# Kernel optimization log

Measured on AMD Instinct MI355X. Metric: run time of the kernel, lower is better.

## Reference

```python
import jax, jax.numpy as jnp
import numpy as np

B, IN_DIM, N_NODES, N_LEAVES, N_ACTIONS = 131072, 128, 511, 512, 16


def setup_inputs() -> dict:
    key = jax.random.key(0)
    k1, k2, k3, k4 = jax.random.split(key, 4)
    x = jax.random.normal(k1, (B, IN_DIM), dtype=jnp.float32)
    W1 = jax.random.normal(k2, (N_NODES, IN_DIM), dtype=jnp.float32) * 0.1
    b1 = jax.random.normal(k3, (N_NODES,), dtype=jnp.float32) * 0.1
    W2 = jax.random.normal(k4, (N_LEAVES, 2 * N_NODES), dtype=jnp.float32) * 0.05
    # leaf -> action assignment; arange % n_actions guarantees every group non-empty
    leaf_actions = (jnp.arange(N_LEAVES) % N_ACTIONS).astype(jnp.int32)
    return {"x": x, "W1": W1, "b1": b1, "W2": W2, "leaf_actions": leaf_actions}


def reference(x, W1, b1, W2, leaf_actions):
    # linear1
    h = x @ W1.T + b1                      # [B, N_NODES]
    # relu(h) || relu(-h)
    z = jnp.concatenate([jax.nn.relu(h), jax.nn.relu(-h)], axis=1)  # [B, 2*N_NODES]
    # linear2 (no bias)
    y = z @ W2.T                           # [B, N_LEAVES]
    # grouped segment-max over leaf columns, grouped by action id
    pooled = jax.ops.segment_max(y.T, leaf_actions, num_segments=N_ACTIONS).T  # [B, N_ACTIONS]
    return jax.nn.softmax(pooled, axis=-1)
```

## Files before the change

kernel.cpp:

```cpp
#include <hip/hip_runtime.h>
#include <hip/hip_bf16.h>

typedef unsigned short u16;
typedef unsigned int u32;
typedef __attribute__((ext_vector_type(8))) short bf16x8;
typedef __attribute__((ext_vector_type(16))) float f32x16;

#define NROWS   131072
#define KDIM    128
#define NNODES  511
#define NACT    16

__device__ __forceinline__ u16 f2b(float v) {
  return __builtin_bit_cast(u16, __float2bfloat16(v));
}

union Frag {
  bf16x8 v;
  u16    u[8];
  int4   i;
  int    d[4];
};

#define Z16 {0.f,0.f,0.f,0.f,0.f,0.f,0.f,0.f,0.f,0.f,0.f,0.f,0.f,0.f,0.f,0.f}

__global__ void prep_k(const float* __restrict__ W1, const float* __restrict__ W2,
                       const float* __restrict__ b1, u16* __restrict__ w1f,
                       u16* __restrict__ wgt, float* __restrict__ b1r) {
  int bid = blockIdx.x, t = threadIdx.x;
  if (bid < 256) {
    int o = bid * 256 + t;
    int j = o & 7, l = (o >> 3) & 63, ks = (o >> 9) & 7, nt = o >> 12;
    int node = nt * 32 + (l & 31);
    int k = ks * 16 + ((l >> 5) << 3) + j;
    w1f[o] = f2b(node < NNODES ? W1[node * KDIM + k] : 0.f);
  } else if (bid < 2304) {
    int o = (bid - 256) * 256 + t;
    int j = o & 7, l = (o >> 3) & 63, lt = (o >> 9) & 15, s = o >> 13;
    int type = s & 1, kstep = s >> 1;
    int leaf = lt * 32 + (l & 31);
    int n = kstep * 16 + ((l >> 5) << 3) + j;
    float va = 0.f, vb = 0.f;
    if (n < NNODES) {
      va = W2[leaf * (2 * NNODES) + n];
      vb = W2[leaf * (2 * NNODES) + NNODES + n];
    }
    wgt[o] = f2b(type ? 0.5f * (va + vb) : 0.5f * (va - vb));
  } else {
    int o = (bid - 2304) * 256 + t;
    int r = o & 15, hi2 = (o >> 4) & 1, nt = o >> 5;
    int node = nt * 32 + (r & 3) + 8 * (r >> 2) + 4 * hi2;
    b1r[o] = (node < NNODES) ? b1[node] : 0.f;
  }
}

__global__ __launch_bounds__(512, 2) void fused_k(const float* __restrict__ x,
                                                  const u16* __restrict__ w1f,
                                                  const u16* __restrict__ wgt,
                                                  const float* __restrict__ b1r,
                                                  float* __restrict__ out) {
  __shared__ u16 Hh[4 * 32 * 64 * 8];
  __shared__ u16 Ss[32 * 64 * 8];

  const int t = threadIdx.x, w = t >> 6, l = t & 63;
  const int la = l & 31, hi = l >> 5;
  const int rg = blockIdx.x;

  {
    const float* xb = x + (size_t)rg * 128 * KDIM;
#pragma unroll
    for (int i = 0; i < 4; ++i) {
      int f = w * 4 + i;
      int rt = f >> 3, ks = f & 7;
      const float* src = xb + (rt * 32 + la) * KDIM + ks * 16 + hi * 8;
      float4 v0 = *(const float4*)src;
      float4 v1 = *(const float4*)(src + 4);
      Frag fr;
      fr.u[0] = f2b(v0.x); fr.u[1] = f2b(v0.y); fr.u[2] = f2b(v0.z); fr.u[3] = f2b(v0.w);
      fr.u[4] = f2b(v1.x); fr.u[5] = f2b(v1.y); fr.u[6] = f2b(v1.z); fr.u[7] = f2b(v1.w);
      *(int4*)&Ss[f * 512 + l * 8] = fr.i;
    }
  }
  __syncthreads();

  {
    const int nt0 = w * 2;
    Frag a1[16];
#pragma unroll
    for (int q = 0; q < 16; ++q)
      a1[q].i = *(const int4*)(w1f + ((size_t)((nt0 + (q >> 3)) * 8 + (q & 7)) * 64 + l) * 8);
    float4 bias[2][4];
#pragma unroll
    for (int n2 = 0; n2 < 2; ++n2)
#pragma unroll
      for (int g = 0; g < 4; ++g)
        bias[n2][g] = *(const float4*)(b1r + ((nt0 + n2) * 2 + hi) * 16 + g * 4);

#pragma unroll 1
    for (int rt = 0; rt < 4; ++rt) {
      f32x16 c0 = Z16, c1 = Z16;
#pragma unroll
      for (int ks = 0; ks < 8; ++ks) {
        Frag b;
        b.i = *(const int4*)&Ss[(rt * 8 + ks) * 512 + l * 8];
        c0 = __builtin_amdgcn_mfma_f32_32x32x16_bf16(a1[ks].v, b.v, c0, 0, 0, 0);
        c1 = __builtin_amdgcn_mfma_f32_32x32x16_bf16(a1[8 + ks].v, b.v, c1, 0, 0, 0);
      }
#pragma unroll
      for (int n2 = 0; n2 < 2; ++n2) {
        int nt = nt0 + n2;
#pragma unroll
        for (int p = 0; p < 8; ++p) {
          int q = p >> 1, e = p & 1;
          int r0 = 4 * q + 2 * e;
          float bv0 = e ? bias[n2][q].z : bias[n2][q].x;
          float bv1 = e ? bias[n2][q].w : bias[n2][q].y;
          float v0 = (n2 ? c1[r0]     : c0[r0])     + bv0;
          float v1 = (n2 ? c1[r0 + 1] : c0[r0 + 1]) + bv1;
          int n32 = 8 * q + 4 * hi + 2 * e;
          int c_h = n32 >> 4, jj = n32 & 15;
          u32 pkv = (u32)f2b(v0) | ((u32)f2b(v1) << 16);
          *(u32*)&Hh[((rt * 32 + nt * 2 + c_h) * 64 + ((jj >> 3) << 5) + la) * 8 + (jj & 6)] = pkv;
        }
      }
    }
  }
  __syncthreads();

  f32x16 acc[4][2] = {{Z16, Z16}, {Z16, Z16}, {Z16, Z16}, {Z16, Z16}};

#define WADDR(k, type, i) (wgt + ((size_t)((k) * 32 + (type) * 16 + w * 2 + (i))) * 512 + l * 8)

  Frag Ad0, Ad1, As0, As1, Bd0, Bd1, Bs0, Bs1;
  Ad0.i = *(const int4*)WADDR(0, 0, 0); Ad1.i = *(const int4*)WADDR(0, 0, 1);
  As0.i = *(const int4*)WADDR(0, 1, 0); As1.i = *(const int4*)WADDR(0, 1, 1);
  Bd0.i = *(const int4*)WADDR(1, 0, 0); Bd1.i = *(const int4*)WADDR(1, 0, 1);
  Bs0.i = *(const int4*)WADDR(1, 1, 0); Bs1.i = *(const int4*)WADDR(1, 1, 1);

#define KSTEP(kk, D0, D1, S0, S1, kpf)                                                            \
  {                                                                                               \
    Frag ha[4];                                                                                   \
    _Pragma("unroll") for (int rt = 0; rt < 4; ++rt)                                              \
      ha[rt].i = *(const int4*)&Hh[((rt * 32 + (kk)) * 64 + l) * 8];                              \
    _Pragma("unroll") for (int rt = 0; rt < 4; ++rt) {                                            \
      acc[rt][0] = __builtin_amdgcn_mfma_f32_32x32x16_bf16(ha[rt].v, D0.v, acc[rt][0], 0, 0, 0);  \
      acc[rt][1] = __builtin_amdgcn_mfma_f32_32x32x16_bf16(ha[rt].v, D1.v, acc[rt][1], 0, 0, 0);  \
    }                                                                                             \
    _Pragma("unroll") for (int rt = 0; rt < 4; ++rt)                                              \
      _Pragma("unroll") for (int d = 0; d < 4; ++d) ha[rt].d[d] &= 0x7FFF7FFF;                    \
    _Pragma("unroll") for (int rt = 0; rt < 4; ++rt) {                                            \
      acc[rt][0] = __builtin_amdgcn_mfma_f32_32x32x16_bf16(ha[rt].v, S0.v, acc[rt][0], 0, 0, 0);  \
      acc[rt][1] = __builtin_amdgcn_mfma_f32_32x32x16_bf16(ha[rt].v, S1.v, acc[rt][1], 0, 0, 0);  \
    }                                                                                             \
    if ((kpf) < 32) {                                                                             \
      D0.i = *(const int4*)WADDR((kpf), 0, 0); D1.i = *(const int4*)WADDR((kpf), 0, 1);           \
      S0.i = *(const int4*)WADDR((kpf), 1, 0); S1.i = *(const int4*)WADDR((kpf), 1, 1);           \
    }                                                                                             \
  }

#pragma unroll 1
  for (int k = 0; k < 32; k += 2) {
    KSTEP(k,     Ad0, Ad1, As0, As1, k + 2);
    KSTEP(k + 1, Bd0, Bd1, Bs0, Bs1, k + 3);
  }

  __syncthreads();

  float* Hred = (float*)Hh;
#pragma unroll
  for (int rt = 0; rt < 4; ++rt)
#pragma unroll
    for (int r = 0; r < 16; ++r) {
      int row = rt * 32 + (r & 3) + 8 * (r >> 2) + 4 * hi;
      float v = fmaxf(acc[rt][0][r], acc[rt][1][r]);
      Hred[(w * 128 + row) * 32 + (la ^ ((r & 3) << 2))] = v;
    }
  __syncthreads();
  {
    int row = t >> 2, ag = t & 3;
    int xr = (row & 3) << 2;
    float p0 = -1e30f, p1 = -1e30f, p2 = -1e30f, p3 = -1e30f;
#pragma unroll
    for (int ww = 0; ww < 8; ++ww)
#pragma unroll
      for (int h2 = 0; h2 < 2; ++h2) {
        float4 v = *(const float4*)&Hred[(ww * 128 + row) * 32 + ((h2 * 16 + ag * 4) ^ xr)];
        p0 = fmaxf(p0, v.x); p1 = fmaxf(p1, v.y);
        p2 = fmaxf(p2, v.z); p3 = fmaxf(p3, v.w);
      }
    float m = fmaxf(fmaxf(p0, p1), fmaxf(p2, p3));
    m = fmaxf(m, __shfl_xor(m, 1));
    m = fmaxf(m, __shfl_xor(m, 2));
    float e0 = __expf(p0 - m), e1 = __expf(p1 - m), e2 = __expf(p2 - m), e3 = __expf(p3 - m);
    float ssum = e0 + e1 + e2 + e3;
    ssum += __shfl_xor(ssum, 1);
    ssum += __shfl_xor(ssum, 2);
    float inv = 1.f / ssum;
    float4 o4;
    o4.x = e0 * inv; o4.y = e1 * inv; o4.z = e2 * inv; o4.w = e3 * inv;
    *(float4*)(out + ((size_t)rg * 128 + row) * NACT + ag * 4) = o4;
  }
}

extern "C" void kernel_launch(void* const* d_in, const int* in_sizes, int n_in,
                              void* d_out, int out_size, void* d_ws, size_t ws_size,
                              hipStream_t stream) {
  const float* x  = (const float*)d_in[0];
  const float* W1 = (const float*)d_in[1];
  const float* b1 = (const float*)d_in[2];
  const float* W2 = (const float*)d_in[3];

  char* ws = (char*)d_ws;
  u16*   w1f = (u16*)ws;
  u16*   wgt = (u16*)(ws + 131072);
  float* b1r = (float*)(ws + 131072 + 1048576);

  prep_k <<<dim3(2308), dim3(256), 0, stream>>>(W1, W2, b1, w1f, wgt, b1r);
  fused_k<<<dim3(NROWS / 128), dim3(512), 0, stream>>>(x, w1f, wgt, b1r, (float*)d_out);
}
```

Measured before the change: 223.0 us.

## Split fused kernel work across 16 waves per 1024-thread block

```diff
diff --git a/kernel.cpp b/kernel.cpp
--- a/kernel.cpp
+++ b/kernel.cpp
@@ -54,11 +54,11 @@
   }
 }
 
-__global__ __launch_bounds__(512, 2) void fused_k(const float* __restrict__ x,
-                                                  const u16* __restrict__ w1f,
-                                                  const u16* __restrict__ wgt,
-                                                  const float* __restrict__ b1r,
-                                                  float* __restrict__ out) {
+__global__ __launch_bounds__(1024, 4) void fused_k(const float* __restrict__ x,
+                                                   const u16* __restrict__ w1f,
+                                                   const u16* __restrict__ wgt,
+                                                   const float* __restrict__ b1r,
+                                                   float* __restrict__ out) {
   __shared__ u16 Hh[4 * 32 * 64 * 8];
   __shared__ u16 Ss[32 * 64 * 8];
 
@@ -69,8 +69,8 @@
   {
     const float* xb = x + (size_t)rg * 128 * KDIM;
 #pragma unroll
-    for (int i = 0; i < 4; ++i) {
-      int f = w * 4 + i;
+    for (int i = 0; i < 2; ++i) {
+      int f = w * 2 + i;
       int rt = f >> 3, ks = f & 7;
       const float* src = xb + (rt * 32 + la) * KDIM + ks * 16 + hi * 8;
       float4 v0 = *(const float4*)src;
@@ -84,84 +84,70 @@
   __syncthreads();
 
   {
-    const int nt0 = w * 2;
-    Frag a1[16];
-#pragma unroll
-    for (int q = 0; q < 16; ++q)
-      a1[q].i = *(const int4*)(w1f + ((size_t)((nt0 + (q >> 3)) * 8 + (q & 7)) * 64 + l) * 8);
-    float4 bias[2][4];
-#pragma unroll
-    for (int n2 = 0; n2 < 2; ++n2)
-#pragma unroll
-      for (int g = 0; g < 4; ++g)
-        bias[n2][g] = *(const float4*)(b1r + ((nt0 + n2) * 2 + hi) * 16 + g * 4);
+    Frag a1[8];
+#pragma unroll
+    for (int q = 0; q < 8; ++q)
+      a1[q].i = *(const int4*)(w1f + ((size_t)(w * 8 + q) * 64 + l) * 8);
+    float4 bias[4];
+#pragma unroll
+    for (int g = 0; g < 4; ++g)
+      bias[g] = *(const float4*)(b1r + (w * 2 + hi) * 16 + g * 4);
 
 #pragma unroll 1
     for (int rt = 0; rt < 4; ++rt) {
-      f32x16 c0 = Z16, c1 = Z16;
+      f32x16 c0 = Z16;
 #pragma unroll
       for (int ks = 0; ks < 8; ++ks) {
         Frag b;
         b.i = *(const int4*)&Ss[(rt * 8 + ks) * 512 + l * 8];
         c0 = __builtin_amdgcn_mfma_f32_32x32x16_bf16(a1[ks].v, b.v, c0, 0, 0, 0);
-        c1 = __builtin_amdgcn_mfma_f32_32x32x16_bf16(a1[8 + ks].v, b.v, c1, 0, 0, 0);
       }
 #pragma unroll
-      for (int n2 = 0; n2 < 2; ++n2) {
-        int nt = nt0 + n2;
-#pragma unroll
-        for (int p = 0; p < 8; ++p) {
-          int q = p >> 1, e = p & 1;
-          int r0 = 4 * q + 2 * e;
-          float bv0 = e ? bias[n2][q].z : bias[n2][q].x;
-          float bv1 = e ? bias[n2][q].w : bias[n2][q].y;
-          float v0 = (n2 ? c1[r0]     : c0[r0])     + bv0;
-          float v1 = (n2 ? c1[r0 + 1] : c0[r0 + 1]) + bv1;
-          int n32 = 8 * q + 4 * hi + 2 * e;
-          int c_h = n32 >> 4, jj = n32 & 15;
-          u32 pkv = (u32)f2b(v0) | ((u32)f2b(v1) << 16);
-          *(u32*)&Hh[((rt * 32 + nt * 2 + c_h) * 64 + ((jj >> 3) << 5) + la) * 8 + (jj & 6)] = pkv;
-        }
+      for (int p = 0; p < 8; ++p) {
+        int q = p >> 1, e = p & 1;
+        int r0 = 4 * q + 2 * e;
+        float bv0 = e ? bias[q].z : bias[q].x;
+        float bv1 = e ? bias[q].w : bias[q].y;
+        float v0 = c0[r0] + bv0;
+        float v1 = c0[r0 + 1] + bv1;
+        int n32 = 8 * q + 4 * hi + 2 * e;
+        int c_h = n32 >> 4, jj = n32 & 15;
+        u32 pkv = (u32)f2b(v0) | ((u32)f2b(v1) << 16);
+        *(u32*)&Hh[((rt * 32 + w * 2 + c_h) * 64 + ((jj >> 3) << 5) + la) * 8 + (jj & 6)] = pkv;
       }
     }
   }
   __syncthreads();
 
-  f32x16 acc[4][2] = {{Z16, Z16}, {Z16, Z16}, {Z16, Z16}, {Z16, Z16}};
-
-#define WADDR(k, type, i) (wgt + ((size_t)((k) * 32 + (type) * 16 + w * 2 + (i))) * 512 + l * 8)
-
-  Frag Ad0, Ad1, As0, As1, Bd0, Bd1, Bs0, Bs1;
-  Ad0.i = *(const int4*)WADDR(0, 0, 0); Ad1.i = *(const int4*)WADDR(0, 0, 1);
-  As0.i = *(const int4*)WADDR(0, 1, 0); As1.i = *(const int4*)WADDR(0, 1, 1);
-  Bd0.i = *(const int4*)WADDR(1, 0, 0); Bd1.i = *(const int4*)WADDR(1, 0, 1);
-  Bs0.i = *(const int4*)WADDR(1, 1, 0); Bs1.i = *(const int4*)WADDR(1, 1, 1);
-
-#define KSTEP(kk, D0, D1, S0, S1, kpf)                                                            \
-  {                                                                                               \
-    Frag ha[4];                                                                                   \
-    _Pragma("unroll") for (int rt = 0; rt < 4; ++rt)                                              \
-      ha[rt].i = *(const int4*)&Hh[((rt * 32 + (kk)) * 64 + l) * 8];                              \
-    _Pragma("unroll") for (int rt = 0; rt < 4; ++rt) {                                            \
-      acc[rt][0] = __builtin_amdgcn_mfma_f32_32x32x16_bf16(ha[rt].v, D0.v, acc[rt][0], 0, 0, 0);  \
-      acc[rt][1] = __builtin_amdgcn_mfma_f32_32x32x16_bf16(ha[rt].v, D1.v, acc[rt][1], 0, 0, 0);  \
-    }                                                                                             \
-    _Pragma("unroll") for (int rt = 0; rt < 4; ++rt)                                              \
-      _Pragma("unroll") for (int d = 0; d < 4; ++d) ha[rt].d[d] &= 0x7FFF7FFF;                    \
-    _Pragma("unroll") for (int rt = 0; rt < 4; ++rt) {                                            \
-      acc[rt][0] = __builtin_amdgcn_mfma_f32_32x32x16_bf16(ha[rt].v, S0.v, acc[rt][0], 0, 0, 0);  \
-      acc[rt][1] = __builtin_amdgcn_mfma_f32_32x32x16_bf16(ha[rt].v, S1.v, acc[rt][1], 0, 0, 0);  \
-    }                                                                                             \
-    if ((kpf) < 32) {                                                                             \
-      D0.i = *(const int4*)WADDR((kpf), 0, 0); D1.i = *(const int4*)WADDR((kpf), 0, 1);           \
-      S0.i = *(const int4*)WADDR((kpf), 1, 0); S1.i = *(const int4*)WADDR((kpf), 1, 1);           \
-    }                                                                                             \
+  f32x16 acc[4] = {Z16, Z16, Z16, Z16};
+
+#define WADDR(k, type) (wgt + ((size_t)((k) * 32 + (type) * 16 + w)) * 512 + l * 8)
+
+  Frag AD, AS, BD, BS;
+  AD.i = *(const int4*)WADDR(0, 0); AS.i = *(const int4*)WADDR(0, 1);
+  BD.i = *(const int4*)WADDR(1, 0); BS.i = *(const int4*)WADDR(1, 1);
+
+#define KSTEP(kk, D, S, kpf)                                                              \
+  {                                                                                       \
+    Frag ha[4];                                                                           \
+    _Pragma("unroll") for (int rt = 0; rt < 4; ++rt)                                      \
+      ha[rt].i = *(const int4*)&Hh[((rt * 32 + (kk)) * 64 + l) * 8];                      \
+    _Pragma("unroll") for (int rt = 0; rt < 4; ++rt)                                      \
+      acc[rt] = __builtin_amdgcn_mfma_f32_32x32x16_bf16(ha[rt].v, D.v, acc[rt], 0, 0, 0); \
+    _Pragma("unroll") for (int rt = 0; rt < 4; ++rt)                                      \
+      _Pragma("unroll") for (int d = 0; d < 4; ++d) ha[rt].d[d] &= 0x7FFF7FFF;            \
+    _Pragma("unroll") for (int rt = 0; rt < 4; ++rt)                                      \
+      acc[rt] = __builtin_amdgcn_mfma_f32_32x32x16_bf16(ha[rt].v, S.v, acc[rt], 0, 0, 0); \
+    if ((kpf) < 32) {                                                                     \
+      D.i = *(const int4*)WADDR((kpf), 0);                                                \
+      S.i = *(const int4*)WADDR((kpf), 1);                                                \
+    }                                                                                     \
   }
 
 #pragma unroll 1
   for (int k = 0; k < 32; k += 2) {
-    KSTEP(k,     Ad0, Ad1, As0, As1, k + 2);
-    KSTEP(k + 1, Bd0, Bd1, Bs0, Bs1, k + 3);
+    KSTEP(k,     AD, AS, k + 2);
+    KSTEP(k + 1, BD, BS, k + 3);
   }
 
   __syncthreads();
@@ -171,34 +157,33 @@
   for (int rt = 0; rt < 4; ++rt)
 #pragma unroll
     for (int r = 0; r < 16; ++r) {
+      float v = acc[rt][r];
+      v = fmaxf(v, __shfl_xor(v, 16));
       int row = rt * 32 + (r & 3) + 8 * (r >> 2) + 4 * hi;
-      float v = fmaxf(acc[rt][0][r], acc[rt][1][r]);
-      Hred[(w * 128 + row) * 32 + (la ^ ((r & 3) << 2))] = v;
+      if (la < 16) Hred[(w * 128 + row) * 16 + la] = v;
     }
   __syncthreads();
   {
-    int row = t >> 2, ag = t & 3;
-    int xr = (row & 3) << 2;
-    float p0 = -1e30f, p1 = -1e30f, p2 = -1e30f, p3 = -1e30f;
-#pragma unroll
-    for (int ww = 0; ww < 8; ++ww)
-#pragma unroll
-      for (int h2 = 0; h2 < 2; ++h2) {
-        float4 v = *(const float4*)&Hred[(ww * 128 + row) * 32 + ((h2 * 16 + ag * 4) ^ xr)];
-        p0 = fmaxf(p0, v.x); p1 = fmaxf(p1, v.y);
-        p2 = fmaxf(p2, v.z); p3 = fmaxf(p3, v.w);
-      }
-    float m = fmaxf(fmaxf(p0, p1), fmaxf(p2, p3));
+    int row = t >> 3, ap = t & 7;
+    float m0 = -1e30f, m1 = -1e30f;
+#pragma unroll
+    for (int ww = 0; ww < 16; ++ww) {
+      m0 = fmaxf(m0, Hred[(ww * 128 + row) * 16 + ap]);
+      m1 = fmaxf(m1, Hred[(ww * 128 + row) * 16 + ap + 8]);
+    }
+    float m = fmaxf(m0, m1);
     m = fmaxf(m, __shfl_xor(m, 1));
     m = fmaxf(m, __shfl_xor(m, 2));
-    float e0 = __expf(p0 - m), e1 = __expf(p1 - m), e2 = __expf(p2 - m), e3 = __expf(p3 - m);
-    float ssum = e0 + e1 + e2 + e3;
-    ssum += __shfl_xor(ssum, 1);
-    ssum += __shfl_xor(ssum, 2);
-    float inv = 1.f / ssum;
-    float4 o4;
-    o4.x = e0 * inv; o4.y = e1 * inv; o4.z = e2 * inv; o4.w = e3 * inv;
-    *(float4*)(out + ((size_t)rg * 128 + row) * NACT + ag * 4) = o4;
+    m = fmaxf(m, __shfl_xor(m, 4));
+    float e0 = __expf(m0 - m), e1 = __expf(m1 - m);
+    float s = e0 + e1;
+    s += __shfl_xor(s, 1);
+    s += __shfl_xor(s, 2);
+    s += __shfl_xor(s, 4);
+    float inv = 1.f / s;
+    float* orow = out + ((size_t)rg * 128 + row) * NACT;
+    orow[ap]     = e0 * inv;
+    orow[ap + 8] = e1 * inv;
   }
 }
 
@@ -216,5 +201,5 @@
   float* b1r = (float*)(ws + 131072 + 1048576);
 
   prep_k <<<dim3(2308), dim3(256), 0, stream>>>(W1, W2, b1, w1f, wgt, b1r);
-  fused_k<<<dim3(NROWS / 128), dim3(512), 0, stream>>>(x, w1f, wgt, b1r, (float*)d_out);
-}
+  fused_k<<<dim3(NROWS / 128), dim3(1024), 0, stream>>>(x, w1f, wgt, b1r, (float*)d_out);
+}
```

New measurement: 250.6 us. 1.12x slower.

## Fuse weight prep into persistent cooperative kernel with grid sync

Applied to the files above, without the earlier changes.

```diff
diff --git a/kernel.cpp b/kernel.cpp
--- a/kernel.cpp
+++ b/kernel.cpp
@@ -1,5 +1,8 @@
 #include <hip/hip_runtime.h>
 #include <hip/hip_bf16.h>
+#include <hip/hip_cooperative_groups.h>
+
+namespace cg = cooperative_groups;
 
 typedef unsigned short u16;
 typedef unsigned int u32;
@@ -54,151 +57,194 @@
   }
 }
 
+template<int COOP>
 __global__ __launch_bounds__(512, 2) void fused_k(const float* __restrict__ x,
-                                                  const u16* __restrict__ w1f,
-                                                  const u16* __restrict__ wgt,
-                                                  const float* __restrict__ b1r,
+                                                  const float* __restrict__ W1,
+                                                  const float* __restrict__ b1,
+                                                  const float* __restrict__ W2,
+                                                  u16* __restrict__ w1f,
+                                                  u16* __restrict__ wgt,
+                                                  float* __restrict__ b1r,
                                                   float* __restrict__ out) {
   __shared__ u16 Hh[4 * 32 * 64 * 8];
   __shared__ u16 Ss[32 * 64 * 8];
 
   const int t = threadIdx.x, w = t >> 6, l = t & 63;
   const int la = l & 31, hi = l >> 5;
-  const int rg = blockIdx.x;
-
-  {
-    const float* xb = x + (size_t)rg * 128 * KDIM;
-#pragma unroll
-    for (int i = 0; i < 4; ++i) {
-      int f = w * 4 + i;
-      int rt = f >> 3, ks = f & 7;
-      const float* src = xb + (rt * 32 + la) * KDIM + ks * 16 + hi * 8;
-      float4 v0 = *(const float4*)src;
-      float4 v1 = *(const float4*)(src + 4);
-      Frag fr;
-      fr.u[0] = f2b(v0.x); fr.u[1] = f2b(v0.y); fr.u[2] = f2b(v0.z); fr.u[3] = f2b(v0.w);
-      fr.u[4] = f2b(v1.x); fr.u[5] = f2b(v1.y); fr.u[6] = f2b(v1.z); fr.u[7] = f2b(v1.w);
-      *(int4*)&Ss[f * 512 + l * 8] = fr.i;
-    }
-  }
-  __syncthreads();
-
-  {
-    const int nt0 = w * 2;
-    Frag a1[16];
-#pragma unroll
-    for (int q = 0; q < 16; ++q)
-      a1[q].i = *(const int4*)(w1f + ((size_t)((nt0 + (q >> 3)) * 8 + (q & 7)) * 64 + l) * 8);
-    float4 bias[2][4];
-#pragma unroll
-    for (int n2 = 0; n2 < 2; ++n2)
-#pragma unroll
-      for (int g = 0; g < 4; ++g)
-        bias[n2][g] = *(const float4*)(b1r + ((nt0 + n2) * 2 + hi) * 16 + g * 4);
+
+  if constexpr (COOP) {
+    int gid = blockIdx.x * 512 + t;
+    for (int i = gid; i < 590848; i += 131072) {
+      if (i < 65536) {
+        int o = i;
+        int j = o & 7, ll = (o >> 3) & 63, ks = (o >> 9) & 7, nt = o >> 12;
+        int node = nt * 32 + (ll & 31);
+        int k2 = ks * 16 + ((ll >> 5) << 3) + j;
+        w1f[o] = f2b(node < NNODES ? W1[node * KDIM + k2] : 0.f);
+      } else if (i < 589824) {
+        int o = i - 65536;
+        int j = o & 7, ll = (o >> 3) & 63, lt = (o >> 9) & 15, s = o >> 13;
+        int type = s & 1, kstep = s >> 1;
+        int leaf = lt * 32 + (ll & 31);
+        int n = kstep * 16 + ((ll >> 5) << 3) + j;
+        float va = 0.f, vb = 0.f;
+        if (n < NNODES) {
+          va = W2[leaf * (2 * NNODES) + n];
+          vb = W2[leaf * (2 * NNODES) + NNODES + n];
+        }
+        wgt[o] = f2b(type ? 0.5f * (va + vb) : 0.5f * (va - vb));
+      } else {
+        int o = i - 589824;
+        int r = o & 15, hi2 = (o >> 4) & 1, nt = o >> 5;
+        int node = nt * 32 + (r & 3) + 8 * (r >> 2) + 4 * hi2;
+        b1r[o] = (node < NNODES) ? b1[node] : 0.f;
+      }
+    }
+    __threadfence();
+    cg::this_grid().sync();
+  }
 
 #pragma unroll 1
-    for (int rt = 0; rt < 4; ++rt) {
-      f32x16 c0 = Z16, c1 = Z16;
-#pragma unroll
-      for (int ks = 0; ks < 8; ++ks) {
-        Frag b;
-        b.i = *(const int4*)&Ss[(rt * 8 + ks) * 512 + l * 8];
-        c0 = __builtin_amdgcn_mfma_f32_32x32x16_bf16(a1[ks].v, b.v, c0, 0, 0, 0);
-        c1 = __builtin_amdgcn_mfma_f32_32x32x16_bf16(a1[8 + ks].v, b.v, c1, 0, 0, 0);
-      }
-#pragma unroll
-      for (int n2 = 0; n2 < 2; ++n2) {
-        int nt = nt0 + n2;
-#pragma unroll
-        for (int p = 0; p < 8; ++p) {
-          int q = p >> 1, e = p & 1;
-          int r0 = 4 * q + 2 * e;
-          float bv0 = e ? bias[n2][q].z : bias[n2][q].x;
-          float bv1 = e ? bias[n2][q].w : bias[n2][q].y;
-          float v0 = (n2 ? c1[r0]     : c0[r0])     + bv0;
-          float v1 = (n2 ? c1[r0 + 1] : c0[r0 + 1]) + bv1;
-          int n32 = 8 * q + 4 * hi + 2 * e;
-          int c_h = n32 >> 4, jj = n32 & 15;
-          u32 pkv = (u32)f2b(v0) | ((u32)f2b(v1) << 16);
-          *(u32*)&Hh[((rt * 32 + nt * 2 + c_h) * 64 + ((jj >> 3) << 5) + la) * 8 + (jj & 6)] = pkv;
-        }
-      }
-    }
-  }
-  __syncthreads();
-
-  f32x16 acc[4][2] = {{Z16, Z16}, {Z16, Z16}, {Z16, Z16}, {Z16, Z16}};
+  for (int rg = blockIdx.x; rg < NROWS / 128; rg += gridDim.x) {
+
+    {
+      const float* xb = x + (size_t)rg * 128 * KDIM;
+#pragma unroll
+      for (int i = 0; i < 4; ++i) {
+        int f = w * 4 + i;
+        int rt = f >> 3, ks = f & 7;
+        const float* src = xb + (rt * 32 + la) * KDIM + ks * 16 + hi * 8;
+        float4 v0 = *(const float4*)src;
+        float4 v1 = *(const float4*)(src + 4);
+        Frag fr;
+        fr.u[0] = f2b(v0.x); fr.u[1] = f2b(v0.y); fr.u[2] = f2b(v0.z); fr.u[3] = f2b(v0.w);
+        fr.u[4] = f2b(v1.x); fr.u[5] = f2b(v1.y); fr.u[6] = f2b(v1.z); fr.u[7] = f2b(v1.w);
+        *(int4*)&Ss[f * 512 + l * 8] = fr.i;
+      }
+    }
+    __syncthreads();
+
+    {
+      const int nt0 = w * 2;
+      Frag a1[16];
+#pragma unroll
+      for (int q = 0; q < 16; ++q)
+        a1[q].i = *(const int4*)(w1f + ((size_t)((nt0 + (q >> 3)) * 8 + (q & 7)) * 64 + l) * 8);
+      float4 bias[2][4];
+#pragma unroll
+      for (int n2 = 0; n2 < 2; ++n2)
+#pragma unroll
+        for (int g = 0; g < 4; ++g)
+          bias[n2][g] = *(const float4*)(b1r + ((nt0 + n2) * 2 + hi) * 16 + g * 4);
+
+#pragma unroll 1
+      for (int rt = 0; rt < 4; ++rt) {
+        f32x16 c0 = Z16, c1 = Z16;
+#pragma unroll
+        for (int ks = 0; ks < 8; ++ks) {
+          Frag b;
+          b.i = *(const int4*)&Ss[(rt * 8 + ks) * 512 + l * 8];
+          c0 = __builtin_amdgcn_mfma_f32_32x32x16_bf16(a1[ks].v, b.v, c0, 0, 0, 0);
+          c1 = __builtin_amdgcn_mfma_f32_32x32x16_bf16(a1[8 + ks].v, b.v, c1, 0, 0, 0);
+        }
+#pragma unroll
+        for (int n2 = 0; n2 < 2; ++n2) {
+          int nt = nt0 + n2;
+#pragma unroll
+          for (int p = 0; p < 8; ++p) {
+            int q = p >> 1, e = p & 1;
+            int r0 = 4 * q + 2 * e;
+            float bv0 = e ? bias[n2][q].z : bias[n2][q].x;
+            float bv1 = e ? bias[n2][q].w : bias[n2][q].y;
+            float v0 = (n2 ? c1[r0]     : c0[r0])     + bv0;
+            float v1 = (n2 ? c1[r0 + 1] : c0[r0 + 1]) + bv1;
+            int n32 = 8 * q + 4 * hi + 2 * e;
+            int c_h = n32 >> 4, jj = n32 & 15;
+            u32 pkv = (u32)f2b(v0) | ((u32)f2b(v1) << 16);
+            *(u32*)&Hh[((rt * 32 + nt * 2 + c_h) * 64 + ((jj >> 3) << 5) + la) * 8 + (jj & 6)] = pkv;
+          }
+        }
+      }
+    }
+    __syncthreads();
+
+    f32x16 acc[4][2] = {{Z16, Z16}, {Z16, Z16}, {Z16, Z16}, {Z16, Z16}};
 
 #define WADDR(k, type, i) (wgt + ((size_t)((k) * 32 + (type) * 16 + w * 2 + (i))) * 512 + l * 8)
 
-  Frag Ad0, Ad1, As0, As1, Bd0, Bd1, Bs0, Bs1;
-  Ad0.i = *(const int4*)WADDR(0, 0, 0); Ad1.i = *(const int4*)WADDR(0, 0, 1);
-  As0.i = *(const int4*)WADDR(0, 1, 0); As1.i = *(const int4*)WADDR(0, 1, 1);
-  Bd0.i = *(const int4*)WADDR(1, 0, 0); Bd1.i = *(const int4*)WADDR(1, 0, 1);
-  Bs0.i = *(const int4*)WADDR(1, 1, 0); Bs1.i = *(const int4*)WADDR(1, 1, 1);
+    Frag Ad0, Ad1, As0, As1, Bd0, Bd1, Bs0, Bs1;
+    Ad0.i = *(const int4*)WADDR(0, 0, 0); Ad1.i = *(const int4*)WADDR(0, 0, 1);
+    As0.i = *(const int4*)WADDR(0, 1, 0); As1.i = *(const int4*)WADDR(0, 1, 1);
+    Bd0.i = *(const int4*)WADDR(1, 0, 0); Bd1.i = *(const int4*)WADDR(1, 0, 1);
+    Bs0.i = *(const int4*)WADDR(1, 1, 0); Bs1.i = *(const int4*)WADDR(1, 1, 1);
 
 #define KSTEP(kk, D0, D1, S0, S1, kpf)                                                            \
-  {                                                                                               \
-    Frag ha[4];                                                                                   \
-    _Pragma("unroll") for (int rt = 0; rt < 4; ++rt)                                              \
-      ha[rt].i = *(const int4*)&Hh[((rt * 32 + (kk)) * 64 + l) * 8];                              \
-    _Pragma("unroll") for (int rt = 0; rt < 4; ++rt) {                                            \
-      acc[rt][0] = __builtin_amdgcn_mfma_f32_32x32x16_bf16(ha[rt].v, D0.v, acc[rt][0], 0, 0, 0);  \
-      acc[rt][1] = __builtin_amdgcn_mfma_f32_32x32x16_bf16(ha[rt].v, D1.v, acc[rt][1], 0, 0, 0);  \
-    }                                                                                             \
-    _Pragma("unroll") for (int rt = 0; rt < 4; ++rt)                                              \
-      _Pragma("unroll") for (int d = 0; d < 4; ++d) ha[rt].d[d] &= 0x7FFF7FFF;                    \
-    _Pragma("unroll") for (int rt = 0; rt < 4; ++rt) {                                            \
-      acc[rt][0] = __builtin_amdgcn_mfma_f32_32x32x16_bf16(ha[rt].v, S0.v, acc[rt][0], 0, 0, 0);  \
-      acc[rt][1] = __builtin_amdgcn_mfma_f32_32x32x16_bf16(ha[rt].v, S1.v, acc[rt][1], 0, 0, 0);  \
-    }                                                                                             \
-    if ((kpf) < 32) {                                                                             \
-      D0.i = *(const int4*)WADDR((kpf), 0, 0); D1.i = *(const int4*)WADDR((kpf), 0, 1);           \
-      S0.i = *(const int4*)WADDR((kpf), 1, 0); S1.i = *(const int4*)WADDR((kpf), 1, 1);           \
-    }                                                                                             \
-  }
+    {                                                                                             \
+      Frag ha[4];                                                                                 \
+      _Pragma("unroll") for (int rt = 0; rt < 4; ++rt)                                            \
+        ha[rt].i = *(const int4*)&Hh[((rt * 32 + (kk)) * 64 + l) * 8];                            \
+      _Pragma("unroll") for (int rt = 0; rt < 4; ++rt) {                                          \
+        acc[rt][0] = __builtin_amdgcn_mfma_f32_32x32x16_bf16(ha[rt].v, D0.v, acc[rt][0], 0, 0, 0);\
+        acc[rt][1] = __builtin_amdgcn_mfma_f32_32x32x16_bf16(ha[rt].v, D1.v, acc[rt][1], 0, 0, 0);\
+      }                                                                                           \
+      _Pragma("unroll") for (int rt = 0; rt < 4; ++rt)                                            \
+        _Pragma("unroll") for (int d = 0; d < 4; ++d) ha[rt].d[d] &= 0x7FFF7FFF;                  \
+      _Pragma("unroll") for (int rt = 0; rt < 4; ++rt) {                                          \
+        acc[rt][0] = __builtin_amdgcn_mfma_f32_32x32x16_bf16(ha[rt].v, S0.v, acc[rt][0], 0, 0, 0);\
+        acc[rt][1] = __builtin_amdgcn_mfma_f32_32x32x16_bf16(ha[rt].v, S1.v, acc[rt][1], 0, 0, 0);\
+      }                                                                                           \
+      if ((kpf) < 32) {                                                                           \
+        D0.i = *(const int4*)WADDR((kpf), 0, 0); D1.i = *(const int4*)WADDR((kpf), 0, 1);         \
+        S0.i = *(const int4*)WADDR((kpf), 1, 0); S1.i = *(const int4*)WADDR((kpf), 1, 1);         \
+      }                                                                                           \
+    }
 
 #pragma unroll 1
-  for (int k = 0; k < 32; k += 2) {
-    KSTEP(k,     Ad0, Ad1, As0, As1, k + 2);
-    KSTEP(k + 1, Bd0, Bd1, Bs0, Bs1, k + 3);
-  }
-
-  __syncthreads();
-
-  float* Hred = (float*)Hh;
-#pragma unroll
-  for (int rt = 0; rt < 4; ++rt)
-#pragma unroll
-    for (int r = 0; r < 16; ++r) {
-      int row = rt * 32 + (r & 3) + 8 * (r >> 2) + 4 * hi;
-      float v = fmaxf(acc[rt][0][r], acc[rt][1][r]);
-      Hred[(w * 128 + row) * 32 + (la ^ ((r & 3) << 2))] = v;
-    }
-  __syncthreads();
-  {
-    int row = t >> 2, ag = t & 3;
-    int xr = (row & 3) << 2;
-    float p0 = -1e30f, p1 = -1e30f, p2 = -1e30f, p3 = -1e30f;
-#pragma unroll
-    for (int ww = 0; ww < 8; ++ww)
-#pragma unroll
-      for (int h2 = 0; h2 < 2; ++h2) {
-        float4 v = *(const float4*)&Hred[(ww * 128 + row) * 32 + ((h2 * 16 + ag * 4) ^ xr)];
-        p0 = fmaxf(p0, v.x); p1 = fmaxf(p1, v.y);
-        p2 = fmaxf(p2, v.z); p3 = fmaxf(p3, v.w);
-      }
-    float m = fmaxf(fmaxf(p0, p1), fmaxf(p2, p3));
-    m = fmaxf(m, __shfl_xor(m, 1));
-    m = fmaxf(m, __shfl_xor(m, 2));
-    float e0 = __expf(p0 - m), e1 = __expf(p1 - m), e2 = __expf(p2 - m), e3 = __expf(p3 - m);
-    float ssum = e0 + e1 + e2 + e3;
-    ssum += __shfl_xor(ssum, 1);
-    ssum += __shfl_xor(ssum, 2);
-    float inv = 1.f / ssum;
-    float4 o4;
-    o4.x = e0 * inv; o4.y = e1 * inv; o4.z = e2 * inv; o4.w = e3 * inv;
-    *(float4*)(out + ((size_t)rg * 128 + row) * NACT + ag * 4) = o4;
+    for (int k = 0; k < 32; k += 2) {
+      KSTEP(k,     Ad0, Ad1, As0, As1, k + 2);
+      KSTEP(k + 1, Bd0, Bd1, Bs0, Bs1, k + 3);
+    }
+#undef KSTEP
+#undef WADDR
+
+    __syncthreads();
+
+    float* Hred = (float*)Hh;
+#pragma unroll
+    for (int rt = 0; rt < 4; ++rt)
+#pragma unroll
+      for (int r = 0; r < 16; ++r) {
+        int row = rt * 32 + (r & 3) + 8 * (r >> 2) + 4 * hi;
+        float v = fmaxf(acc[rt][0][r], acc[rt][1][r]);
+        v = fmaxf(v, __shfl_xor(v, 16));
+        Hred[(w * 128 + row) * 32 + (la ^ ((r & 3) << 2))] = v;
+      }
+    __syncthreads();
+    {
+      int row = t >> 2, ag = t & 3;
+      int xr = (row & 3) << 2;
+      float p0 = -1e30f, p1 = -1e30f, p2 = -1e30f, p3 = -1e30f;
+#pragma unroll
+      for (int ww = 0; ww < 8; ++ww)
+#pragma unroll
+        for (int h2 = 0; h2 < 2; ++h2) {
+          float4 v = *(const float4*)&Hred[(ww * 128 + row) * 32 + ((h2 * 16 + ag * 4) ^ xr)];
+          p0 = fmaxf(p0, v.x); p1 = fmaxf(p1, v.y);
+          p2 = fmaxf(p2, v.z); p3 = fmaxf(p3, v.w);
+        }
+      float m = fmaxf(fmaxf(p0, p1), fmaxf(p2, p3));
+      m = fmaxf(m, __shfl_xor(m, 1));
+      m = fmaxf(m, __shfl_xor(m, 2));
+      float e0 = __expf(p0 - m), e1 = __expf(p1 - m), e2 = __expf(p2 - m), e3 = __expf(p3 - m);
+      float ssum = e0 + e1 + e2 + e3;
+      ssum += __shfl_xor(ssum, 1);
+      ssum += __shfl_xor(ssum, 2);
+      float inv = 1.f / ssum;
+      float4 o4;
+      o4.x = e0 * inv; o4.y = e1 * inv; o4.z = e2 * inv; o4.w = e3 * inv;
+      *(float4*)(out + ((size_t)rg * 128 + row) * NACT + ag * 4) = o4;
+    }
+    __syncthreads();
   }
 }
 
@@ -214,7 +260,15 @@
   u16*   w1f = (u16*)ws;
   u16*   wgt = (u16*)(ws + 131072);
   float* b1r = (float*)(ws + 131072 + 1048576);
-
-  prep_k <<<dim3(2308), dim3(256), 0, stream>>>(W1, W2, b1, w1f, wgt, b1r);
-  fused_k<<<dim3(NROWS / 128), dim3(512), 0, stream>>>(x, w1f, wgt, b1r, (float*)d_out);
-}
+  float* outp = (float*)d_out;
+
+  void* args[] = {(void*)&x, (void*)&W1, (void*)&b1, (void*)&W2,
+                  (void*)&w1f, (void*)&wgt, (void*)&b1r, (void*)&outp};
+  hipError_t err = hipLaunchCooperativeKernel((const void*)fused_k<1>,
+                                              dim3(256), dim3(512), args, 0, stream);
+  if (err != hipSuccess) {
+    (void)hipGetLastError();
+    prep_k<<<dim3(2308), dim3(256), 0, stream>>>(W1, W2, b1, w1f, wgt, b1r);
+    fused_k<0><<<dim3(1024), dim3(512), 0, stream>>>(x, W1, b1, W2, w1f, wgt, b1r, outp);
+  }
+}
```

Result: slower. 296.3 us (+32.9%).

## Double-buffer LDS activation fragments, stagger per-wave K start, raise MFMA priority

Applied to the files above, without the earlier changes.

```diff
diff --git a/kernel.cpp b/kernel.cpp
--- a/kernel.cpp
+++ b/kernel.cpp
@@ -129,40 +129,54 @@
 
   f32x16 acc[4][2] = {{Z16, Z16}, {Z16, Z16}, {Z16, Z16}, {Z16, Z16}};
 
-#define WADDR(k, type, i) (wgt + ((size_t)((k) * 32 + (type) * 16 + w * 2 + (i))) * 512 + l * 8)
-
+#define WADDR(k, type, i) (wgt + ((size_t)((((k) & 31) * 32 + (type) * 16 + w * 2 + (i))) * 512) + l * 8)
+
+#define LDHA(BUF, kk)                                                                     \
+  { _Pragma("unroll") for (int rt = 0; rt < 4; ++rt)                                      \
+      BUF[rt].i = *(const int4*)&Hh[((rt * 32 + ((kk) & 31)) * 64 + l) * 8]; }
+
+#define MFCL(HA, D0, D1, S0, S1)                                                          \
+  {                                                                                       \
+    __builtin_amdgcn_s_setprio(1);                                                        \
+    _Pragma("unroll") for (int rt = 0; rt < 4; ++rt) {                                    \
+      acc[rt][0] = __builtin_amdgcn_mfma_f32_32x32x16_bf16(HA[rt].v, D0.v, acc[rt][0], 0, 0, 0); \
+      acc[rt][1] = __builtin_amdgcn_mfma_f32_32x32x16_bf16(HA[rt].v, D1.v, acc[rt][1], 0, 0, 0); \
+    }                                                                                     \
+    _Pragma("unroll") for (int rt = 0; rt < 4; ++rt)                                      \
+      _Pragma("unroll") for (int d = 0; d < 4; ++d) HA[rt].d[d] &= 0x7FFF7FFF;            \
+    _Pragma("unroll") for (int rt = 0; rt < 4; ++rt) {                                    \
+      acc[rt][0] = __builtin_amdgcn_mfma_f32_32x32x16_bf16(HA[rt].v, S0.v, acc[rt][0], 0, 0, 0); \
+      acc[rt][1] = __builtin_amdgcn_mfma_f32_32x32x16_bf16(HA[rt].v, S1.v, acc[rt][1], 0, 0, 0); \
+    }                                                                                     \
+    __builtin_amdgcn_s_setprio(0);                                                        \
+  }
+
+  const int k0 = (w * 4) & 31;
+
+  Frag haA[4], haB[4];
   Frag Ad0, Ad1, As0, As1, Bd0, Bd1, Bs0, Bs1;
-  Ad0.i = *(const int4*)WADDR(0, 0, 0); Ad1.i = *(const int4*)WADDR(0, 0, 1);
-  As0.i = *(const int4*)WADDR(0, 1, 0); As1.i = *(const int4*)WADDR(0, 1, 1);
-  Bd0.i = *(const int4*)WADDR(1, 0, 0); Bd1.i = *(const int4*)WADDR(1, 0, 1);
-  Bs0.i = *(const int4*)WADDR(1, 1, 0); Bs1.i = *(const int4*)WADDR(1, 1, 1);
-
-#define KSTEP(kk, D0, D1, S0, S1, kpf)                                                            \
-  {                                                                                               \
-    Frag ha[4];                                                                                   \
-    _Pragma("unroll") for (int rt = 0; rt < 4; ++rt)                                              \
-      ha[rt].i = *(const int4*)&Hh[((rt * 32 + (kk)) * 64 + l) * 8];                              \
-    _Pragma("unroll") for (int rt = 0; rt < 4; ++rt) {                                            \
-      acc[rt][0] = __builtin_amdgcn_mfma_f32_32x32x16_bf16(ha[rt].v, D0.v, acc[rt][0], 0, 0, 0);  \
-      acc[rt][1] = __builtin_amdgcn_mfma_f32_32x32x16_bf16(ha[rt].v, D1.v, acc[rt][1], 0, 0, 0);  \
-    }                                                                                             \
-    _Pragma("unroll") for (int rt = 0; rt < 4; ++rt)                                              \
-      _Pragma("unroll") for (int d = 0; d < 4; ++d) ha[rt].d[d] &= 0x7FFF7FFF;                    \
-    _Pragma("unroll") for (int rt = 0; rt < 4; ++rt) {                                            \
-      acc[rt][0] = __builtin_amdgcn_mfma_f32_32x32x16_bf16(ha[rt].v, S0.v, acc[rt][0], 0, 0, 0);  \
-      acc[rt][1] = __builtin_amdgcn_mfma_f32_32x32x16_bf16(ha[rt].v, S1.v, acc[rt][1], 0, 0, 0);  \
-    }                                                                                             \
-    if ((kpf) < 32) {                                                                             \
-      D0.i = *(const int4*)WADDR((kpf), 0, 0); D1.i = *(const int4*)WADDR((kpf), 0, 1);           \
-      S0.i = *(const int4*)WADDR((kpf), 1, 0); S1.i = *(const int4*)WADDR((kpf), 1, 1);           \
-    }                                                                                             \
-  }
+
+  LDHA(haA, k0);
+  Ad0.i = *(const int4*)WADDR(k0, 0, 0);     Ad1.i = *(const int4*)WADDR(k0, 0, 1);
+  As0.i = *(const int4*)WADDR(k0, 1, 0);     As1.i = *(const int4*)WADDR(k0, 1, 1);
+  Bd0.i = *(const int4*)WADDR(k0 + 1, 0, 0); Bd1.i = *(const int4*)WADDR(k0 + 1, 0, 1);
+  Bs0.i = *(const int4*)WADDR(k0 + 1, 1, 0); Bs1.i = *(const int4*)WADDR(k0 + 1, 1, 1);
 
 #pragma unroll 1
-  for (int k = 0; k < 32; k += 2) {
-    KSTEP(k,     Ad0, Ad1, As0, As1, k + 2);
-    KSTEP(k + 1, Bd0, Bd1, Bs0, Bs1, k + 3);
-  }
+  for (int ki = 0; ki < 32; ki += 2) {
+    int k = k0 + ki;
+    LDHA(haB, k + 1);
+    MFCL(haA, Ad0, Ad1, As0, As1);
+    Ad0.i = *(const int4*)WADDR(k + 2, 0, 0); Ad1.i = *(const int4*)WADDR(k + 2, 0, 1);
+    As0.i = *(const int4*)WADDR(k + 2, 1, 0); As1.i = *(const int4*)WADDR(k + 2, 1, 1);
+    LDHA(haA, k + 2);
+    MFCL(haB, Bd0, Bd1, Bs0, Bs1);
+    Bd0.i = *(const int4*)WADDR(k + 3, 0, 0); Bd1.i = *(const int4*)WADDR(k + 3, 0, 1);
+    Bs0.i = *(const int4*)WADDR(k + 3, 1, 0); Bs1.i = *(const int4*)WADDR(k + 3, 1, 1);
+  }
+#undef MFCL
+#undef LDHA
+#undef WADDR
 
   __syncthreads();
 
@@ -173,6 +187,7 @@
     for (int r = 0; r < 16; ++r) {
       int row = rt * 32 + (r & 3) + 8 * (r >> 2) + 4 * hi;
       float v = fmaxf(acc[rt][0][r], acc[rt][1][r]);
+      v = fmaxf(v, __shfl_xor(v, 16));
       Hred[(w * 128 + row) * 32 + (la ^ ((r & 3) << 2))] = v;
     }
   __syncthreads();
```

Result: slower. 236.0 us (+5.8%).
